# Optimization experiments

Measured on AMD Instinct MI355X. Metric: run time of the kernel, lower is better.

## Reference

```python
import jax, jax.numpy as jnp
import numpy as np
import math

D_MODEL = 256
N_HEADS = 4
D_K = D_MODEL // N_HEADS
N_LAYERS = 4
PAD_ID = 0
LN_EPS = 1e-5


def _posenc(seq_len, d_model):
    pos = jnp.arange(seq_len, dtype=jnp.float32)[:, None]
    div = jnp.exp(jnp.arange(0, d_model, 2, dtype=jnp.float32) * (-math.log(10000.0) / d_model))
    pe = jnp.zeros((seq_len, d_model), dtype=jnp.float32)
    pe = pe.at[:, 0::2].set(jnp.sin(pos * div))
    pe = pe.at[:, 1::2].set(jnp.cos(pos * div))
    return pe  # (S, D)


def _layernorm(x, g, b):
    mu = jnp.mean(x, axis=-1, keepdims=True)
    var = jnp.mean((x - mu) ** 2, axis=-1, keepdims=True)
    return (x - mu) / jnp.sqrt(var + LN_EPS) * g + b


def _attention(x, mask_b11s, Wq, bq, Wk, bk, Wv, bv, Wo, bo):
    B, S, D = x.shape
    q = (x @ Wq + bq).reshape(B, S, N_HEADS, D_K)
    k = (x @ Wk + bk).reshape(B, S, N_HEADS, D_K)
    v = (x @ Wv + bv).reshape(B, S, N_HEADS, D_K)
    scores = jnp.einsum('bqhd,bkhd->bhqk', q, k) / math.sqrt(D_K)
    scores = jnp.where(mask_b11s, scores, -jnp.inf)
    attn = jax.nn.softmax(scores, axis=-1)
    out = jnp.einsum('bhqk,bkhd->bqhd', attn, v).reshape(B, S, D)
    return out @ Wo + bo


def setup_inputs() -> dict:
    key = jax.random.key(0)
    ks = jax.random.split(key, 16)
    B, S, V, D, F, L, C = 16, 2048, 32, D_MODEL, 1024, N_LAYERS, 10
    input_ids = jax.random.randint(ks[0], (B, S), 0, V, dtype=jnp.int64)
    emb = jax.random.normal(ks[1], (V, D), jnp.float32) * (D ** -0.5)
    emb = emb.at[PAD_ID].set(0.0)  # padding_idx
    sc = 0.05
    inp = {
        'input_ids': input_ids,
        'emb': emb,
        'Wq': jax.random.normal(ks[2], (L, D, D), jnp.float32) * sc,
        'bq': jnp.zeros((L, D), jnp.float32),
        'Wk': jax.random.normal(ks[3], (L, D, D), jnp.float32) * sc,
        'bk': jnp.zeros((L, D), jnp.float32),
        'Wv': jax.random.normal(ks[4], (L, D, D), jnp.float32) * sc,
        'bv': jnp.zeros((L, D), jnp.float32),
        'Wo': jax.random.normal(ks[5], (L, D, D), jnp.float32) * sc,
        'bo': jnp.zeros((L, D), jnp.float32),
        'g1': jnp.ones((L, D), jnp.float32),
        'be1': jnp.zeros((L, D), jnp.float32),
        'W1': jax.random.normal(ks[6], (L, D, F), jnp.float32) * sc,
        'b1': jnp.zeros((L, F), jnp.float32),
        'W2': jax.random.normal(ks[7], (L, F, D), jnp.float32) * sc,
        'b2': jnp.zeros((L, D), jnp.float32),
        'g2': jnp.ones((L, D), jnp.float32),
        'be2': jnp.zeros((L, D), jnp.float32),
        'Wc': jax.random.normal(ks[8], (D, C), jnp.float32) * sc,
        'bc': jnp.zeros((C,), jnp.float32),
    }
    return inp


def reference(input_ids, emb, Wq, bq, Wk, bk, Wv, bv, Wo, bo,
              g1, be1, W1, b1, W2, b2, g2, be2, Wc, bc):
    B, S = input_ids.shape
    attn_mask = (input_ids != PAD_ID)                      # (B, S) bool
    mask_b11s = attn_mask[:, None, None, :]                # (B,1,1,S)
    x = emb[input_ids] * math.sqrt(D_MODEL)                # (B,S,D)
    x = x + _posenc(S, D_MODEL)[None]
    for l in range(N_LAYERS):
        a = _attention(x, mask_b11s, Wq[l], bq[l], Wk[l], bk[l], Wv[l], bv[l], Wo[l], bo[l])
        x = _layernorm(x + a, g1[l], be1[l])
        ff = jax.nn.relu(x @ W1[l] + b1[l]) @ W2[l] + b2[l]
        x = _layernorm(x + ff, g2[l], be2[l])
    # mean pooling over non-pad tokens
    m = attn_mask.astype(jnp.float32)[:, :, None]          # (B,S,1)
    pooled = jnp.sum(x * m, axis=1) / jnp.clip(jnp.sum(m, axis=1), 1e-9)
    logits = pooled @ Wc + bc                              # (B, num_classes)
    return logits
```

## Files before the change

### kernel.cpp

```cpp
#include <hip/hip_runtime.h>
#include <hip/hip_bf16.h>
#include <math.h>

#define D_MODEL 256
#define NHEADS 4
#define DK 64
#define NLAYERS 4
#define FFDIM 1024
#define BB 16
#define SS 2048
#define NTOK (BB*SS)

#define QSCALE 0.18033688011112042f
#define MASKNEG -30000.0f

typedef __attribute__((ext_vector_type(8))) short bf16x8;
typedef __attribute__((ext_vector_type(4))) short s16x4;
typedef __attribute__((ext_vector_type(4))) float f32x4;

__device__ __forceinline__ short f2bf(float f) {
    __hip_bfloat16 h = __float2bfloat16(f);
    return *reinterpret_cast<short*>(&h);
}

__global__ void embed_kernel(const int* __restrict__ ids, const float* __restrict__ emb,
                             float* __restrict__ x, short* __restrict__ xb) {
    int idx = blockIdx.x * 256 + threadIdx.x;
    int tok = idx >> 8;
    int d   = idx & 255;
    int s   = tok & (SS - 1);
    int id  = ids[tok];
    float e = emb[id * D_MODEL + d] * 16.0f;
    float i2 = (float)((d >> 1) << 1);
    float div = expf(i2 * (-9.210340371976184f / 256.0f));
    float ang = (float)s * div;
    float pe = (d & 1) ? cosf(ang) : sinf(ang);
    float val = e + pe;
    x[idx] = val;
    xb[idx] = f2bf(val);
}

__global__ void wprep_kernel(const float* __restrict__ Wq, const float* __restrict__ Wk,
                             const float* __restrict__ Wv, const float* __restrict__ Wo,
                             const float* __restrict__ W1, const float* __restrict__ W2,
                             short* __restrict__ wqkv, short* __restrict__ wto,
                             short* __restrict__ w1t, short* __restrict__ w2t) {
    int wid = blockIdx.y, l = blockIdx.z, tile = blockIdx.x;
    int K = (wid == 5) ? 1024 : 256;
    int M = (wid == 4) ? 1024 : 256;
    int tiles = (K >> 6) * (M >> 6);
    if (tile >= tiles) return;
    const float* src; short* dst;
    float scale = (wid == 0) ? QSCALE : 1.0f;
    switch (wid) {
        case 0: src = Wq; dst = wqkv + (size_t)l*196608;            break;
        case 1: src = Wk; dst = wqkv + (size_t)l*196608 + 65536;    break;
        case 2: src = Wv; dst = wqkv + (size_t)l*196608 + 131072;   break;
        case 3: src = Wo; dst = wto + (size_t)l*65536;              break;
        case 4: src = W1; dst = w1t + (size_t)l*262144;             break;
        default: src = W2; dst = w2t + (size_t)l*262144;            break;
    }
    src += (size_t)l * K * M;
    int tm = tile % (M >> 6), tk = tile / (M >> 6);

    __shared__ short t_s[64][68];
    int tid = threadIdx.x;
    #pragma unroll
    for (int u = 0; u < 16; ++u) {
        int e = tid + u * 256;
        int r = e >> 6, c = e & 63;
        t_s[c][r] = f2bf(src[(size_t)(tk*64 + r) * M + tm*64 + c] * scale);
    }
    __syncthreads();
    #pragma unroll
    for (int u = 0; u < 4; ++u) {
        int e = tid + u * 256;
        int r = e >> 4, c4 = (e & 15) * 4;
        s16x4 v;
        v[0] = t_s[r][c4]; v[1] = t_s[r][c4+1]; v[2] = t_s[r][c4+2]; v[3] = t_s[r][c4+3];
        *(s16x4*)&dst[(size_t)(tm*64 + r) * K + tk*64 + c4] = v;
    }
}

__global__ void bprep_kernel(const float* __restrict__ bq, const float* __restrict__ bk,
                             const float* __restrict__ bv, float* __restrict__ bqkv) {
    int idx = blockIdx.x * 256 + threadIdx.x;
    if (idx >= NLAYERS * 768) return;
    int l = idx / 768, j = idx % 768;
    float v;
    if (j < 256) v = bq[l*256 + j] * QSCALE;
    else if (j < 512) v = bk[l*256 + j - 256];
    else v = bv[l*256 + j - 512];
    bqkv[idx] = v;
}

template<int RELU, int VSPLIT>
__global__ __launch_bounds__(256) void gemm_bf16_kernel(
        const short* __restrict__ A, const short* __restrict__ Wt,
        const float* __restrict__ bias, short* __restrict__ Cout,
        short* __restrict__ vt, int N, int K, int M) {
    __shared__ short A_s[128][72];
    __shared__ short B_s[128][72];
    int tid = threadIdx.x;
    int w = tid >> 6, lane = tid & 63;
    int lr = lane & 15, lg = lane >> 4;
    int wr = w >> 1, wc = w & 1;
    int rowBase = blockIdx.x * 128;
    int colBase = blockIdx.y * 128;

    f32x4 acc[4][4];
    #pragma unroll
    for (int m = 0; m < 4; ++m)
        #pragma unroll
        for (int n = 0; n < 4; ++n)
            acc[m][n] = (f32x4){0.f, 0.f, 0.f, 0.f};

    for (int kt = 0; kt < K; kt += 64) {
        #pragma unroll
        for (int u = 0; u < 4; ++u) {
            int e = tid + u * 256;
            int r = e >> 3, c8 = (e & 7) * 8;
            *(bf16x8*)&A_s[r][c8] = *(const bf16x8*)(A + (size_t)(rowBase + r) * K + kt + c8);
        }
        #pragma unroll
        for (int u = 0; u < 4; ++u) {
            int e = tid + u * 256;
            int r = e >> 3, c8 = (e & 7) * 8;
            *(bf16x8*)&B_s[r][c8] = *(const bf16x8*)(Wt + (size_t)(colBase + r) * K + kt + c8);
        }
        __syncthreads();
        #pragma unroll
        for (int ks = 0; ks < 2; ++ks) {
            bf16x8 af[4], bfr[4];
            #pragma unroll
            for (int m = 0; m < 4; ++m)
                af[m] = *(const bf16x8*)&A_s[wr*64 + m*16 + lr][ks*32 + lg*8];
            #pragma unroll
            for (int n = 0; n < 4; ++n)
                bfr[n] = *(const bf16x8*)&B_s[wc*64 + n*16 + lr][ks*32 + lg*8];
            #pragma unroll
            for (int m = 0; m < 4; ++m)
                #pragma unroll
                for (int n = 0; n < 4; ++n)
                    acc[m][n] = __builtin_amdgcn_mfma_f32_16x16x32_bf16(af[m], bfr[n], acc[m][n], 0, 0, 0);
        }
        __syncthreads();
    }

    #pragma unroll
    for (int m = 0; m < 4; ++m) {
        int row = rowBase + wr*64 + m*16 + lg*4;
        #pragma unroll
        for (int n = 0; n < 4; ++n) {
            int col = colBase + wc*64 + n*16 + lr;
            float bv = bias[col];
            if (VSPLIT && col >= 512) {
                int hh = (col - 512) >> 6, dl = (col - 512) & 63;
                int bb = row >> 11, s0 = row & 2047;
                s16x4 ow;
                #pragma unroll
                for (int r = 0; r < 4; ++r) ow[r] = f2bf(acc[m][n][r] + bv);
                *(s16x4*)&vt[((size_t)(bb * NHEADS + hh) * DK + dl) * SS + s0] = ow;
            } else {
                #pragma unroll
                for (int r = 0; r < 4; ++r) {
                    float vv = acc[m][n][r] + bv;
                    if (RELU) vv = fmaxf(vv, 0.0f);
                    Cout[(size_t)(row + r) * M + col] = f2bf(vv);
                }
            }
        }
    }
}

__global__ __launch_bounds__(256) void gemm_ln_kernel(
        const short* __restrict__ A, const short* __restrict__ Wt,
        const float* __restrict__ bias, const float* __restrict__ resid,
        const float* __restrict__ g, const float* __restrict__ be,
        float* __restrict__ xf, short* __restrict__ xb, int K) {
    __shared__ short A_s[64][72];
    __shared__ short B_s[256][72];
    __shared__ float red_s[2][4][64];
    __shared__ float mu_s[64], rs_s[64];
    int tid = threadIdx.x;
    int w = tid >> 6, lane = tid & 63;
    int lr = lane & 15, lg = lane >> 4;
    int rowBase = blockIdx.x * 64;
    int colW = w * 64;

    f32x4 acc[4][4];
    #pragma unroll
    for (int m = 0; m < 4; ++m)
        #pragma unroll
        for (int n = 0; n < 4; ++n)
            acc[m][n] = (f32x4){0.f, 0.f, 0.f, 0.f};

    for (int kt = 0; kt < K; kt += 64) {
        #pragma unroll
        for (int u = 0; u < 2; ++u) {
            int e = tid + u * 256;
            int r = e >> 3, c8 = (e & 7) * 8;
            *(bf16x8*)&A_s[r][c8] = *(const bf16x8*)(A + (size_t)(rowBase + r) * K + kt + c8);
        }
        #pragma unroll
        for (int u = 0; u < 8; ++u) {
            int e = tid + u * 256;
            int r = e >> 3, c8 = (e & 7) * 8;
            *(bf16x8*)&B_s[r][c8] = *(const bf16x8*)(Wt + (size_t)r * K + kt + c8);
        }
        __syncthreads();
        #pragma unroll
        for (int ks = 0; ks < 2; ++ks) {
            bf16x8 af[4], bfr[4];
            #pragma unroll
            for (int m = 0; m < 4; ++m)
                af[m] = *(const bf16x8*)&A_s[m*16 + lr][ks*32 + lg*8];
            #pragma unroll
            for (int n = 0; n < 4; ++n)
                bfr[n] = *(const bf16x8*)&B_s[colW + n*16 + lr][ks*32 + lg*8];
            #pragma unroll
            for (int m = 0; m < 4; ++m)
                #pragma unroll
                for (int n = 0; n < 4; ++n)
                    acc[m][n] = __builtin_amdgcn_mfma_f32_16x16x32_bf16(af[m], bfr[n], acc[m][n], 0, 0, 0);
        }
        __syncthreads();
    }

    #pragma unroll
    for (int m = 0; m < 4; ++m) {
        #pragma unroll
        for (int n = 0; n < 4; ++n) {
            int col = colW + n*16 + lr;
            float bv = bias[col];
            #pragma unroll
            for (int r = 0; r < 4; ++r) {
                int row = rowBase + m*16 + lg*4 + r;
                acc[m][n][r] += bv + resid[(size_t)row * 256 + col];
            }
        }
    }
    #pragma unroll
    for (int m = 0; m < 4; ++m) {
        #pragma unroll
        for (int r = 0; r < 4; ++r) {
            float sum = acc[m][0][r] + acc[m][1][r] + acc[m][2][r] + acc[m][3][r];
            float sq  = acc[m][0][r]*acc[m][0][r] + acc[m][1][r]*acc[m][1][r]
                      + acc[m][2][r]*acc[m][2][r] + acc[m][3][r]*acc[m][3][r];
            #pragma unroll
            for (int off = 1; off < 16; off <<= 1) {
                sum += __shfl_xor(sum, off);
                sq  += __shfl_xor(sq, off);
            }
            if (lr == 0) {
                red_s[0][w][m*16 + lg*4 + r] = sum;
                red_s[1][w][m*16 + lg*4 + r] = sq;
            }
        }
    }
    __syncthreads();
    if (tid < 64) {
        float s = red_s[0][0][tid] + red_s[0][1][tid] + red_s[0][2][tid] + red_s[0][3][tid];
        float q = red_s[1][0][tid] + red_s[1][1][tid] + red_s[1][2][tid] + red_s[1][3][tid];
        float mu = s * (1.0f/256.0f);
        float var = q * (1.0f/256.0f) - mu*mu;
        mu_s[tid] = mu;
        rs_s[tid] = rsqrtf(var + 1e-5f);
    }
    __syncthreads();
    #pragma unroll
    for (int m = 0; m < 4; ++m) {
        #pragma unroll
        for (int n = 0; n < 4; ++n) {
            int col = colW + n*16 + lr;
            float gv = g[col], bev = be[col];
            #pragma unroll
            for (int r = 0; r < 4; ++r) {
                int rloc = m*16 + lg*4 + r;
                int row = rowBase + rloc;
                float o = (acc[m][n][r] - mu_s[rloc]) * rs_s[rloc] * gv + bev;
                xf[(size_t)row * 256 + col] = o;
                xb[(size_t)row * 256 + col] = f2bf(o);
            }
        }
    }
}

__global__ __launch_bounds__(256) void flash_mfma_kernel(
        const short* __restrict__ qkv, const short* __restrict__ vt_g,
        const int* __restrict__ ids, short* __restrict__ out) {
    __shared__ short k_s[64][72];
    __shared__ short vt_s[64][72];
    __shared__ short p_s[4][32][72];
    __shared__ float madd_s[64];

    int bid = blockIdx.x;
    int work = (bid & 7) * 128 + (bid >> 3);
    int qb = work & 15, h = (work >> 4) & 3, b = work >> 6;

    int tid = threadIdx.x;
    int w = tid >> 6, lane = tid & 63;
    int lr = lane & 15, lg = lane >> 4;
    int g = lr >> 2;

    const short* qp = qkv + (size_t)b * SS * 768 + h * DK;
    const short* kp = qp + 256;
    const short* vtp = vt_g + (size_t)(b * NHEADS + h) * DK * SS;

    bf16x8 qf[2][2];
    #pragma unroll
    for (int s = 0; s < 2; ++s) {
        int qrow = qb*128 + w*32 + s*16 + lr;
        #pragma unroll
        for (int ks = 0; ks < 2; ++ks)
            qf[s][ks] = *(const bf16x8*)(qp + (size_t)qrow * 768 + lg*8 + ks*32);
    }

    f32x4 o[2][4];
    float m_i[2] = {-1e30f, -1e30f}, l_i[2] = {0.0f, 0.0f};
    #pragma unroll
    for (int s = 0; s < 2; ++s)
        #pragma unroll
        for (int dt = 0; dt < 4; ++dt)
            o[s][dt] = (f32x4){0.f, 0.f, 0.f, 0.f};

    int r0 = tid >> 3, c8 = (tid & 7) * 8;

    bf16x8 kr[2], vr[2];
    int idv = 1;
    #pragma unroll
    for (int u = 0; u < 2; ++u) {
        kr[u] = *(const bf16x8*)(kp + (size_t)(r0 + u*32) * 768 + c8);
        vr[u] = *(const bf16x8*)(vtp + (size_t)(r0 + u*32) * SS + c8);
    }
    if (tid < 64) idv = ids[b*SS + tid];

    for (int kb = 0; kb < SS/64; ++kb) {
        __syncthreads();
        #pragma unroll
        for (int u = 0; u < 2; ++u) {
            *(bf16x8*)&k_s[r0 + u*32][c8] = kr[u];
            *(bf16x8*)&vt_s[r0 + u*32][c8] = vr[u];
        }
        if (tid < 64)
            madd_s[tid] = (idv != 0) ? 0.0f : MASKNEG;
        if (kb + 1 < SS/64) {
            #pragma unroll
            for (int u = 0; u < 2; ++u) {
                kr[u] = *(const bf16x8*)(kp + (size_t)((kb+1)*64 + r0 + u*32) * 768 + c8);
                vr[u] = *(const bf16x8*)(vtp + (size_t)(r0 + u*32) * SS + (kb+1)*64 + c8);
            }
            if (tid < 64) idv = ids[b*SS + (kb+1)*64 + tid];
        }
        __syncthreads();

        f32x4 madd4[4];
        #pragma unroll
        for (int t = 0; t < 4; ++t)
            madd4[t] = *(const f32x4*)&madd_s[16*t + 4*lg];

        f32x4 sc[2][4];
        __builtin_amdgcn_s_setprio(1);
        #pragma unroll
        for (int t = 0; t < 4; ++t) {
            bf16x8 kf0 = *(const bf16x8*)&k_s[t*16 + lr][lg*8];
            bf16x8 kf1 = *(const bf16x8*)&k_s[t*16 + lr][lg*8 + 32];
            #pragma unroll
            for (int s = 0; s < 2; ++s) {
                f32x4 a = __builtin_amdgcn_mfma_f32_16x16x32_bf16(kf0, qf[s][0], madd4[t], 0, 0, 0);
                a = __builtin_amdgcn_mfma_f32_16x16x32_bf16(kf1, qf[s][1], a, 0, 0, 0);
                sc[s][t] = a;
            }
        }
        __builtin_amdgcn_s_setprio(0);

        #pragma unroll
        for (int s = 0; s < 2; ++s) {
            float mx = sc[s][0][0];
            #pragma unroll
            for (int t = 0; t < 4; ++t)
                #pragma unroll
                for (int r = 0; r < 4; ++r)
                    mx = fmaxf(mx, sc[s][t][r]);
            mx = fmaxf(mx, __shfl_xor(mx, 16));
            mx = fmaxf(mx, __shfl_xor(mx, 32));

            if (!__all(mx <= m_i[s])) {
                float mnew = fmaxf(m_i[s], mx);
                float alpha = __builtin_amdgcn_exp2f(m_i[s] - mnew);
                l_i[s] *= alpha;
                #pragma unroll
                for (int dt = 0; dt < 4; ++dt) o[s][dt] *= alpha;
                m_i[s] = mnew;
            }

            float rsum = 0.0f;
            float pv[4][4];
            #pragma unroll
            for (int t = 0; t < 4; ++t)
                #pragma unroll
                for (int r = 0; r < 4; ++r) {
                    float p = __builtin_amdgcn_exp2f(sc[s][t][r] - m_i[s]);
                    pv[t][r] = p;
                    rsum += p;
                }
            rsum += __shfl_xor(rsum, 16);
            rsum += __shfl_xor(rsum, 32);
            l_i[s] += rsum;

            #pragma unroll
            for (int t = 0; t < 4; ++t) {
                s16x4 pw;
                #pragma unroll
                for (int r = 0; r < 4; ++r) pw[r] = f2bf(pv[t][r]);
                *(s16x4*)&p_s[w][s*16 + lr][16*(t ^ g) + 4*lg] = pw;
            }
        }

        bf16x8 pa[2][2];
        #pragma unroll
        for (int s = 0; s < 2; ++s)
            #pragma unroll
            for (int ks = 0; ks < 2; ++ks) {
                int t0 = 2*ks + (lg >> 1);
                pa[s][ks] = *(const bf16x8*)&p_s[w][s*16 + lr][16*(t0 ^ g) + 8*(lg & 1)];
            }
        __builtin_amdgcn_s_setprio(1);
        #pragma unroll
        for (int dt = 0; dt < 4; ++dt) {
            #pragma unroll
            for (int ks = 0; ks < 2; ++ks) {
                bf16x8 va = *(const bf16x8*)&vt_s[dt*16 + lr][ks*32 + lg*8];
                o[0][dt] = __builtin_amdgcn_mfma_f32_16x16x32_bf16(va, pa[0][ks], o[0][dt], 0, 0, 0);
                o[1][dt] = __builtin_amdgcn_mfma_f32_16x16x32_bf16(va, pa[1][ks], o[1][dt], 0, 0, 0);
            }
        }
        __builtin_amdgcn_s_setprio(0);
    }

    #pragma unroll
    for (int s = 0; s < 2; ++s) {
        float inv = 1.0f / l_i[s];
        int row = b*SS + qb*128 + w*32 + s*16 + lr;
        #pragma unroll
        for (int dt = 0; dt < 4; ++dt) {
            s16x4 ow;
            #pragma unroll
            for (int r = 0; r < 4; ++r) ow[r] = f2bf(o[s][dt][r] * inv);
            *(s16x4*)&out[(size_t)row * 256 + h*DK + dt*16 + 4*lg] = ow;
        }
    }
}

__global__ void pool1_kernel(const float* __restrict__ x, const int* __restrict__ ids,
                             float* __restrict__ partial) {
    int b = blockIdx.x >> 4, chunk = blockIdx.x & 15;
    int d = threadIdx.x;
    float acc = 0.0f;
    int s0 = chunk * 128;
    for (int s = s0; s < s0 + 128; ++s) {
        if (ids[b*SS + s] != 0) acc += x[(size_t)(b*SS + s) * D_MODEL + d];
    }
    partial[(size_t)(b*16 + chunk) * D_MODEL + d] = acc;
}

__global__ void pool2_kernel(const float* __restrict__ partial, const int* __restrict__ ids,
                             float* __restrict__ pooled) {
    int b = blockIdx.x;
    int d = threadIdx.x;
    float acc = 0.0f;
    for (int c = 0; c < 16; ++c) acc += partial[(size_t)(b*16 + c) * D_MODEL + d];
    int cnt = 0;
    for (int s = threadIdx.x; s < SS; s += 256) cnt += (ids[b*SS + s] != 0);
    __shared__ int cs[256];
    cs[threadIdx.x] = cnt;
    __syncthreads();
    for (int off = 128; off > 0; off >>= 1) {
        if (threadIdx.x < off) cs[threadIdx.x] += cs[threadIdx.x + off];
        __syncthreads();
    }
    float total = (float)cs[0];
    pooled[b * D_MODEL + d] = acc / fmaxf(total, 1e-9f);
}

__global__ void cls_kernel(const float* __restrict__ pooled, const float* __restrict__ Wc,
                           const float* __restrict__ bc, float* __restrict__ outp) {
    int t = threadIdx.x;
    if (t >= BB * 10) return;
    int b = t / 10, c = t % 10;
    float acc = bc[c];
    for (int d = 0; d < D_MODEL; ++d)
        acc += pooled[b * D_MODEL + d] * Wc[d * 10 + c];
    outp[t] = acc;
}

extern "C" void kernel_launch(void* const* d_in, const int* in_sizes, int n_in,
                              void* d_out, int out_size, void* d_ws, size_t ws_size,
                              hipStream_t stream) {
    const int*   ids = (const int*)  d_in[0];
    const float* emb = (const float*)d_in[1];
    const float* Wq  = (const float*)d_in[2];
    const float* bq  = (const float*)d_in[3];
    const float* Wk  = (const float*)d_in[4];
    const float* bk  = (const float*)d_in[5];
    const float* Wv  = (const float*)d_in[6];
    const float* bv  = (const float*)d_in[7];
    const float* Wo  = (const float*)d_in[8];
    const float* bo  = (const float*)d_in[9];
    const float* g1  = (const float*)d_in[10];
    const float* be1 = (const float*)d_in[11];
    const float* W1  = (const float*)d_in[12];
    const float* b1  = (const float*)d_in[13];
    const float* W2  = (const float*)d_in[14];
    const float* b2  = (const float*)d_in[15];
    const float* g2  = (const float*)d_in[16];
    const float* be2 = (const float*)d_in[17];
    const float* Wc  = (const float*)d_in[18];
    const float* bc  = (const float*)d_in[19];
    float* outp = (float*)d_out;

    const size_t TD = (size_t)NTOK * D_MODEL;
    float* ws   = (float*)d_ws;
    float* x    = ws;
    short* sb   = (short*)(ws + TD);
    short* xb   = sb;
    short* qkv  = sb + TD;
    short* t0   = sb + 4*TD;
    short* vt_g = sb + 5*TD;
    short* hh   = qkv;
    short* wqkv = sb + 6*TD;
    short* wto  = wqkv + (size_t)NLAYERS*196608;
    short* w1t  = wto  + (size_t)NLAYERS*65536;
    short* w2t  = w1t  + (size_t)NLAYERS*262144;
    float* bqkv = (float*)(w2t + (size_t)NLAYERS*262144);
    float* poolp = bqkv + NLAYERS*768;
    float* pooled = poolp + 65536;

    wprep_kernel<<<dim3(64, 6, NLAYERS), 256, 0, stream>>>(Wq, Wk, Wv, Wo, W1, W2,
                                                           wqkv, wto, w1t, w2t);
    bprep_kernel<<<12, 256, 0, stream>>>(bq, bk, bv, bqkv);
    embed_kernel<<<NTOK, 256, 0, stream>>>(ids, emb, x, xb);

    dim3 gQKV(NTOK/128, 768/128);
    dim3 gF1 (NTOK/128, FFDIM/128);

    for (int l = 0; l < NLAYERS; ++l) {
        gemm_bf16_kernel<0,1><<<gQKV, 256, 0, stream>>>(xb, wqkv + (size_t)l*196608, bqkv + l*768,
                                                        qkv, vt_g, NTOK, D_MODEL, 768);
        flash_mfma_kernel<<<1024, 256, 0, stream>>>(qkv, vt_g, ids, t0);
        gemm_ln_kernel<<<NTOK/64, 256, 0, stream>>>(t0, wto + (size_t)l*65536, bo + l*D_MODEL,
                                                    x, g1 + l*D_MODEL, be1 + l*D_MODEL,
                                                    x, xb, D_MODEL);
        gemm_bf16_kernel<1,0><<<gF1, 256, 0, stream>>>(xb, w1t + (size_t)l*262144, b1 + l*FFDIM,
                                                       hh, nullptr, NTOK, D_MODEL, FFDIM);
        gemm_ln_kernel<<<NTOK/64, 256, 0, stream>>>(hh, w2t + (size_t)l*262144, b2 + l*D_MODEL,
                                                    x, g2 + l*D_MODEL, be2 + l*D_MODEL,
                                                    x, xb, FFDIM);
    }

    pool1_kernel<<<BB*16, 256, 0, stream>>>(x, ids, poolp);
    pool2_kernel<<<BB, 256, 0, stream>>>(poolp, ids, pooled);
    cls_kernel<<<1, 256, 0, stream>>>(pooled, Wc, bc, outp);
}
```

Measured before the change: 1.085 ms.

## Use direct global-to-LDS loads with XOR swizzle in GEMMs; trim attention softmax

Both GEMM kernels now stage A and B tiles through global_load_lds instead of going through registers. The tiles are stored unpadded with an XOR swizzle to avoid LDS bank conflicts, which also shrinks shared memory use. In attention, the per-tile row-sum shuffles are deferred so each lane keeps a partial sum that is reduced once at the end, and the max uses a tree reduction. The P scratch buffer is halved and reused per half-tile. The direct-to-LDS path depends on the lane-to-address mapping matching the swizzle, and reusing the P buffer adds a read-after-write dependency within each wave.

```diff
diff --git a/kernel.cpp b/kernel.cpp
--- a/kernel.cpp
+++ b/kernel.cpp
@@ -21,6 +21,11 @@
 __device__ __forceinline__ short f2bf(float f) {
     __hip_bfloat16 h = __float2bfloat16(f);
     return *reinterpret_cast<short*>(&h);
+}
+
+__device__ __forceinline__ void gl_lds16(const void* g, void* l) {
+    __builtin_amdgcn_global_load_lds((const __attribute__((address_space(1))) void*)g,
+                                     (__attribute__((address_space(3))) void*)l, 16, 0, 0);
 }
 
 __global__ void embed_kernel(const int* __restrict__ ids, const float* __restrict__ emb,
@@ -99,8 +104,8 @@
         const short* __restrict__ A, const short* __restrict__ Wt,
         const float* __restrict__ bias, short* __restrict__ Cout,
         short* __restrict__ vt, int N, int K, int M) {
-    __shared__ short A_s[128][72];
-    __shared__ short B_s[128][72];
+    __shared__ short A_s[128][64];
+    __shared__ short B_s[128][64];
     int tid = threadIdx.x;
     int w = tid >> 6, lane = tid & 63;
     int lr = lane & 15, lg = lane >> 4;
@@ -108,6 +113,9 @@
     int rowBase = blockIdx.x * 128;
     int colBase = blockIdx.y * 128;
 
+    int rS = tid >> 3;
+    int cS = (tid & 7) * 8;
+
     f32x4 acc[4][4];
     #pragma unroll
     for (int m = 0; m < 4; ++m)
@@ -115,29 +123,29 @@
         for (int n = 0; n < 4; ++n)
             acc[m][n] = (f32x4){0.f, 0.f, 0.f, 0.f};
 
+    int fcol = 0;
+
     for (int kt = 0; kt < K; kt += 64) {
         #pragma unroll
         for (int u = 0; u < 4; ++u) {
-            int e = tid + u * 256;
-            int r = e >> 3, c8 = (e & 7) * 8;
-            *(bf16x8*)&A_s[r][c8] = *(const bf16x8*)(A + (size_t)(rowBase + r) * K + kt + c8);
-        }
-        #pragma unroll
-        for (int u = 0; u < 4; ++u) {
-            int e = tid + u * 256;
-            int r = e >> 3, c8 = (e & 7) * 8;
-            *(bf16x8*)&B_s[r][c8] = *(const bf16x8*)(Wt + (size_t)(colBase + r) * K + kt + c8);
+            int r = rS + u * 32;
+            int srcc = cS ^ ((r & 7) << 3);
+            gl_lds16(A + (size_t)(rowBase + r) * K + kt + srcc,
+                     &A_s[0][0] + (size_t)(u * 256 + w * 64) * 8);
+            gl_lds16(Wt + (size_t)(colBase + r) * K + kt + srcc,
+                     &B_s[0][0] + (size_t)(u * 256 + w * 64) * 8);
         }
         __syncthreads();
         #pragma unroll
         for (int ks = 0; ks < 2; ++ks) {
+            int col = (ks*32 + lg*8) ^ ((lr & 7) << 3);
             bf16x8 af[4], bfr[4];
             #pragma unroll
             for (int m = 0; m < 4; ++m)
-                af[m] = *(const bf16x8*)&A_s[wr*64 + m*16 + lr][ks*32 + lg*8];
+                af[m] = *(const bf16x8*)&A_s[wr*64 + m*16 + lr][col];
             #pragma unroll
             for (int n = 0; n < 4; ++n)
-                bfr[n] = *(const bf16x8*)&B_s[wc*64 + n*16 + lr][ks*32 + lg*8];
+                bfr[n] = *(const bf16x8*)&B_s[wc*64 + n*16 + lr][col];
             #pragma unroll
             for (int m = 0; m < 4; ++m)
                 #pragma unroll
@@ -146,6 +154,7 @@
         }
         __syncthreads();
     }
+    (void)fcol;
 
     #pragma unroll
     for (int m = 0; m < 4; ++m) {
@@ -178,8 +187,8 @@
         const float* __restrict__ bias, const float* __restrict__ resid,
         const float* __restrict__ g, const float* __restrict__ be,
         float* __restrict__ xf, short* __restrict__ xb, int K) {
-    __shared__ short A_s[64][72];
-    __shared__ short B_s[256][72];
+    __shared__ short A_s[64][64];
+    __shared__ short B_s[256][64];
     __shared__ float red_s[2][4][64];
     __shared__ float mu_s[64], rs_s[64];
     int tid = threadIdx.x;
@@ -188,6 +197,9 @@
     int rowBase = blockIdx.x * 64;
     int colW = w * 64;
 
+    int rS = tid >> 3;
+    int cS = (tid & 7) * 8;
+
     f32x4 acc[4][4];
     #pragma unroll
     for (int m = 0; m < 4; ++m)
@@ -198,26 +210,29 @@
     for (int kt = 0; kt < K; kt += 64) {
         #pragma unroll
         for (int u = 0; u < 2; ++u) {
-            int e = tid + u * 256;
-            int r = e >> 3, c8 = (e & 7) * 8;
-            *(bf16x8*)&A_s[r][c8] = *(const bf16x8*)(A + (size_t)(rowBase + r) * K + kt + c8);
+            int r = rS + u * 32;
+            int srcc = cS ^ ((r & 7) << 3);
+            gl_lds16(A + (size_t)(rowBase + r) * K + kt + srcc,
+                     &A_s[0][0] + (size_t)(u * 256 + w * 64) * 8);
         }
         #pragma unroll
         for (int u = 0; u < 8; ++u) {
-            int e = tid + u * 256;
-            int r = e >> 3, c8 = (e & 7) * 8;
-            *(bf16x8*)&B_s[r][c8] = *(const bf16x8*)(Wt + (size_t)r * K + kt + c8);
+            int r = rS + u * 32;
+            int srcc = cS ^ ((r & 7) << 3);
+            gl_lds16(Wt + (size_t)r * K + kt + srcc,
+                     &B_s[0][0] + (size_t)(u * 256 + w * 64) * 8);
         }
         __syncthreads();
         #pragma unroll
         for (int ks = 0; ks < 2; ++ks) {
+            int col = (ks*32 + lg*8) ^ ((lr & 7) << 3);
             bf16x8 af[4], bfr[4];
             #pragma unroll
             for (int m = 0; m < 4; ++m)
-                af[m] = *(const bf16x8*)&A_s[m*16 + lr][ks*32 + lg*8];
+                af[m] = *(const bf16x8*)&A_s[m*16 + lr][col];
             #pragma unroll
             for (int n = 0; n < 4; ++n)
-                bfr[n] = *(const bf16x8*)&B_s[colW + n*16 + lr][ks*32 + lg*8];
+                bfr[n] = *(const bf16x8*)&B_s[colW + n*16 + lr][col];
             #pragma unroll
             for (int m = 0; m < 4; ++m)
                 #pragma unroll
@@ -291,7 +306,7 @@
         const int* __restrict__ ids, short* __restrict__ out) {
     __shared__ short k_s[64][72];
     __shared__ short vt_s[64][72];
-    __shared__ short p_s[4][32][72];
+    __shared__ short p_s[4][16][72];
     __shared__ float madd_s[64];
 
     int bid = blockIdx.x;
@@ -374,14 +389,14 @@
         }
         __builtin_amdgcn_s_setprio(0);
 
+        bf16x8 pa[2][2];
         #pragma unroll
         for (int s = 0; s < 2; ++s) {
-            float mx = sc[s][0][0];
-            #pragma unroll
-            for (int t = 0; t < 4; ++t)
-                #pragma unroll
-                for (int r = 0; r < 4; ++r)
-                    mx = fmaxf(mx, sc[s][t][r]);
+            float mt0 = fmaxf(fmaxf(sc[s][0][0], sc[s][0][1]), fmaxf(sc[s][0][2], sc[s][0][3]));
+            float mt1 = fmaxf(fmaxf(sc[s][1][0], sc[s][1][1]), fmaxf(sc[s][1][2], sc[s][1][3]));
+            float mt2 = fmaxf(fmaxf(sc[s][2][0], sc[s][2][1]), fmaxf(sc[s][2][2], sc[s][2][3]));
+            float mt3 = fmaxf(fmaxf(sc[s][3][0], sc[s][3][1]), fmaxf(sc[s][3][2], sc[s][3][3]));
+            float mx = fmaxf(fmaxf(mt0, mt1), fmaxf(mt2, mt3));
             mx = fmaxf(mx, __shfl_xor(mx, 16));
             mx = fmaxf(mx, __shfl_xor(mx, 32));
 
@@ -394,37 +409,32 @@
                 m_i[s] = mnew;
             }
 
-            float rsum = 0.0f;
             float pv[4][4];
             #pragma unroll
             for (int t = 0; t < 4; ++t)
                 #pragma unroll
-                for (int r = 0; r < 4; ++r) {
-                    float p = __builtin_amdgcn_exp2f(sc[s][t][r] - m_i[s]);
-                    pv[t][r] = p;
-                    rsum += p;
-                }
-            rsum += __shfl_xor(rsum, 16);
-            rsum += __shfl_xor(rsum, 32);
-            l_i[s] += rsum;
+                for (int r = 0; r < 4; ++r)
+                    pv[t][r] = __builtin_amdgcn_exp2f(sc[s][t][r] - m_i[s]);
+            float st0 = (pv[0][0] + pv[0][1]) + (pv[0][2] + pv[0][3]);
+            float st1 = (pv[1][0] + pv[1][1]) + (pv[1][2] + pv[1][3]);
+            float st2 = (pv[2][0] + pv[2][1]) + (pv[2][2] + pv[2][3]);
+            float st3 = (pv[3][0] + pv[3][1]) + (pv[3][2] + pv[3][3]);
+            l_i[s] += (st0 + st1) + (st2 + st3);
 
             #pragma unroll
             for (int t = 0; t < 4; ++t) {
                 s16x4 pw;
                 #pragma unroll
                 for (int r = 0; r < 4; ++r) pw[r] = f2bf(pv[t][r]);
-                *(s16x4*)&p_s[w][s*16 + lr][16*(t ^ g) + 4*lg] = pw;
-            }
-        }
-
-        bf16x8 pa[2][2];
-        #pragma unroll
-        for (int s = 0; s < 2; ++s)
+                *(s16x4*)&p_s[w][lr][16*(t ^ g) + 4*lg] = pw;
+            }
             #pragma unroll
             for (int ks = 0; ks < 2; ++ks) {
                 int t0 = 2*ks + (lg >> 1);
-                pa[s][ks] = *(const bf16x8*)&p_s[w][s*16 + lr][16*(t0 ^ g) + 8*(lg & 1)];
-            }
+                pa[s][ks] = *(const bf16x8*)&p_s[w][lr][16*(t0 ^ g) + 8*(lg & 1)];
+            }
+        }
+
         __builtin_amdgcn_s_setprio(1);
         #pragma unroll
         for (int dt = 0; dt < 4; ++dt) {
@@ -440,7 +450,10 @@
 
     #pragma unroll
     for (int s = 0; s < 2; ++s) {
-        float inv = 1.0f / l_i[s];
+        float l = l_i[s];
+        l += __shfl_xor(l, 16);
+        l += __shfl_xor(l, 32);
+        float inv = 1.0f / l;
         int row = b*SS + qb*128 + w*32 + s*16 + lr;
         #pragma unroll
         for (int dt = 0; dt < 4; ++dt) {
```

Result: slower. 1.258 ms (+16.0%).
